# Kernel tuning notes

Measured on AMD Instinct MI355X. Metric: run time of the kernel, lower is better.

## Reference

```python
import jax, jax.numpy as jnp
import numpy as np

B, N, E = 4, 512, 128
NODE_F, EDGE_F, DYN_F, L = 16, 8, 6, 3
TOT_F = NODE_F + DYN_F  # 22


def setup_inputs() -> dict:
    key = jax.random.key(0)
    ks = jax.random.split(key, 20)
    s = 0.05
    return {
        "node_features": jax.random.normal(ks[0], (B, N, NODE_F), jnp.float32),
        "edge_features": jax.random.normal(ks[1], (B, N, N, EDGE_F), jnp.float32),
        "W": jax.random.normal(ks[2], (B, N, N), jnp.float32),
        "assigned": jax.random.randint(ks[3], (B, N), 0, 2) > 0,
        "open_group": jax.random.randint(ks[4], (B, N), 0, 2) > 0,
        "action_mask": jax.random.randint(ks[5], (B, N), 0, 2) > 0,
        "build_limit": jax.random.uniform(ks[6], (B, 3), jnp.float32, 0.5, 2.0),
        "open_group_size": jax.random.uniform(ks[7], (B, 3), jnp.float32, 0.0, 2.0),
        "node_embed_w": jax.random.normal(ks[8], (TOT_F, E), jnp.float32) * s,
        "node_embed_b": jnp.zeros((E,), jnp.float32),
        "mp_node_w": jax.random.normal(ks[9], (L, E, E), jnp.float32) * s,
        "mp_edge_w": jax.random.normal(ks[10], (L, EDGE_F, E), jnp.float32) * s,
        "mp_weight_w": jax.random.normal(ks[11], (L, E), jnp.float32) * s,
        "mp_out_w": jax.random.normal(ks[12], (L, E, E), jnp.float32) * s,
        "mp_out_b": jnp.zeros((L, E), jnp.float32),
        "context_w": jax.random.normal(ks[13], (E, E), jnp.float32) * s,
        "key_w": jax.random.normal(ks[14], (E, E), jnp.float32) * s,
        "logit_bias": jnp.zeros((1,), jnp.float32),
    }


def _policy_logits(node_features, edge_features, W, build_limit, open_group_size,
                   node_embed_w, node_embed_b, mp_node_w, mp_edge_w, mp_weight_w,
                   mp_out_w, mp_out_b, context_w, key_w, logit_bias,
                   assigned, open_group, action_mask):
    # --- dynamic node features: [B,N,6] ---
    ratio = open_group_size / jnp.maximum(build_limit, 1e-6)  # [B,3]
    dyn = jnp.concatenate([
        assigned.astype(jnp.float32)[..., None],
        open_group.astype(jnp.float32)[..., None],
        action_mask.astype(jnp.float32)[..., None],
        jnp.broadcast_to(ratio[:, None, :], (node_features.shape[0], node_features.shape[1], 3)),
    ], axis=-1)
    x = jnp.concatenate([node_features, dyn], axis=-1)  # [B,N,22]
    h = x @ node_embed_w + node_embed_b  # [B,N,E]

    # --- edge-aware message passing, residual per layer ---
    for l in range(L):
        hi = h @ mp_node_w[l]  # [B,N,E]
        ej = jnp.einsum('bijf,fe->bije', edge_features, mp_edge_w[l])  # [B,N,N,E]
        wij = W[..., None] * mp_weight_w[l]  # [B,N,N,E]
        msg = jnp.tanh(hi[:, :, None, :] + ej + wij)  # [B,N,N,E]
        agg = msg.mean(axis=2)  # [B,N,E]
        h = h + agg @ mp_out_w[l] + mp_out_b[l]

    # --- context attention logits ---
    og = open_group.astype(jnp.float32)
    has_open = jnp.any(open_group, axis=-1, keepdims=True)  # [B,1]
    denom = jnp.maximum(og.sum(axis=-1, keepdims=True), 1.0)  # [B,1]
    group_mean = (h * og[..., None]).sum(axis=1) / denom  # [B,E]
    sep_emb = h[:, 0, :]
    context = jnp.where(has_open, group_mean, sep_emb)  # [B,E]
    query = context @ context_w  # [B,E]
    keys = h @ key_w  # [B,N,E]
    logits = jnp.einsum('be,bne->bn', query, keys) / jnp.sqrt(jnp.float32(h.shape[-1]))
    logits = logits + logit_bias[0]
    logits = jnp.where(action_mask, logits, -1e9)
    return logits


def reference(node_features, edge_features, W, assigned, open_group, action_mask,
              build_limit, open_group_size, node_embed_w, node_embed_b,
              mp_node_w, mp_edge_w, mp_weight_w, mp_out_w, mp_out_b,
              context_w, key_w, logit_bias):
    return _policy_logits(node_features, edge_features, W, build_limit, open_group_size,
                          node_embed_w, node_embed_b, mp_node_w, mp_edge_w, mp_weight_w,
                          mp_out_w, mp_out_b, context_w, key_w, logit_bias,
                          assigned, open_group, action_mask)
```

## Files before the change

kernel.cpp:

```cpp
#include <hip/hip_runtime.h>
#include <math.h>

#define BB 4
#define NN 512
#define EE 128
#define NODE_F 16
#define EDGE_F 8
#define LL 3

typedef __attribute__((ext_vector_type(8))) short bf16x8;
typedef __attribute__((ext_vector_type(4))) float f32x4;

__device__ __forceinline__ ushort bf_hi(float x) {
    uint u = __float_as_uint(x);
    return (ushort)((u + 0x7fffu + ((u >> 16) & 1u)) >> 16);
}
__device__ __forceinline__ float bf_f(ushort h) {
    return __uint_as_float(((uint)h) << 16);
}

__global__ __launch_bounds__(512) void k_rows(
    const float* __restrict__ nf,
    const float* __restrict__ ef,
    const float* __restrict__ W,
    const int*   __restrict__ assigned,
    const int*   __restrict__ open_group,
    const int*   __restrict__ action_mask,
    const float* __restrict__ build_limit,
    const float* __restrict__ open_group_size,
    const float* __restrict__ embed_w,
    const float* __restrict__ embed_b,
    const float* __restrict__ node_w,
    const float* __restrict__ edge_w,
    const float* __restrict__ weight_w,
    const float* __restrict__ out_w,
    const float* __restrict__ out_b,
    float* __restrict__ hout)
{
    const int i   = blockIdx.x;
    const int b   = blockIdx.y;
    const int t   = threadIdx.x;
    const int l   = t & 63;
    const int w   = t >> 6;
    const int row = b * NN + i;

    __shared__ bf16x8 afr[32 * 64];
    __shared__ float hsh[EE];
    __shared__ float hish[EE];
    __shared__ float aggfin[EE];
    __shared__ float xsh[24];

    if (t < NODE_F) {
        xsh[t] = nf[row * NODE_F + t];
    } else if (t == 16) {
        xsh[16] = assigned[row] ? 1.0f : 0.0f;
    } else if (t == 17) {
        xsh[17] = open_group[row] ? 1.0f : 0.0f;
    } else if (t == 18) {
        xsh[18] = action_mask[row] ? 1.0f : 0.0f;
    } else if (t < 22) {
        int k = t - 19;
        xsh[t] = open_group_size[b * 3 + k] / fmaxf(build_limit[b * 3 + k], 1e-6f);
    }

    {
        const float* efr = ef + (size_t)row * NN * EDGE_F;
        const float* Wr  = W + (size_t)row * NN;
        #pragma unroll
        for (int q = 0; q < 4; ++q) {
            const int eid = t + 512 * q;
            const int ll  = eid & 63;
            const int jt  = eid >> 6;
            const int g   = ll >> 4;
            const int jj  = jt * 16 + (ll & 15);
            bf16x8 frag;
            if (g < 3) {
                const float4 a = *(const float4*)&efr[jj * 8];
                const float4 c4 = *(const float4*)&efr[jj * 8 + 4];
                float v[8] = {a.x, a.y, a.z, a.w, c4.x, c4.y, c4.z, c4.w};
                if (g < 2) {
                    #pragma unroll
                    for (int m = 0; m < 8; ++m) frag[m] = (short)bf_hi(v[m]);
                } else {
                    #pragma unroll
                    for (int m = 0; m < 8; ++m) {
                        ushort h = bf_hi(v[m]);
                        frag[m] = (short)bf_hi(v[m] - bf_f(h));
                    }
                }
            } else {
                float wv = Wr[jj];
                ushort h = bf_hi(wv);
                ushort lo = bf_hi(wv - bf_f(h));
                frag = (bf16x8){(short)h, (short)h, (short)lo, 0, 0, 0, 0, 0};
            }
            afr[eid] = frag;
        }
    }
    __syncthreads();

    if (t < EE) {
        float h0 = embed_b[t];
        #pragma unroll
        for (int k = 0; k < 22; ++k)
            h0 = fmaf(xsh[k], embed_w[k * EE + t], h0);
        hsh[t] = h0;
    }

    const float c  = 2.8853900817779268f;
    const int  le  = l & 15;
    const int  g   = l >> 4;
    const int  eN  = w * 16 + le;

    for (int lay = 0; lay < LL; ++lay) {
        __syncthreads();

        if (t < EE) {
            const float* nw = node_w + lay * EE * EE + t;
            float hp = 0.0f;
            #pragma unroll 8
            for (int k = 0; k < EE; ++k)
                hp = fmaf(hsh[k], nw[k * EE], hp);
            hish[t] = c * hp;
        }

        bf16x8 bfrag;
        if (g == 3) {
            float x = c * weight_w[lay * EE + eN];
            ushort h = bf_hi(x);
            ushort lo = bf_hi(x - bf_f(h));
            bfrag = (bf16x8){(short)h, (short)lo, (short)h, 0, 0, 0, 0, 0};
        } else {
            const float* ewp = edge_w + lay * EDGE_F * EE + eN;
            if (g == 1) {
                #pragma unroll
                for (int m = 0; m < 8; ++m) {
                    float x = c * ewp[m * EE];
                    ushort h = bf_hi(x);
                    bfrag[m] = (short)bf_hi(x - bf_f(h));
                }
            } else {
                #pragma unroll
                for (int m = 0; m < 8; ++m)
                    bfrag[m] = (short)bf_hi(c * ewp[m * EE]);
            }
        }
        __syncthreads();

        const float hq = hish[eN];
        const f32x4 cin = {hq, hq, hq, hq};

        f32x4 rsum = {0.0f, 0.0f, 0.0f, 0.0f};
        #pragma unroll 4
        for (int jt = 0; jt < 32; ++jt) {
            bf16x8 a = afr[jt * 64 + l];
            f32x4 acc = __builtin_amdgcn_mfma_f32_16x16x32_bf16(a, bfrag, cin, 0, 0, 0);
            #pragma unroll
            for (int r = 0; r < 4; ++r) {
                float ex = __builtin_amdgcn_exp2f(acc[r]);
                rsum[r] += __builtin_amdgcn_rcpf(ex + 1.0f);
            }
        }
        float s = (rsum[0] + rsum[1]) + (rsum[2] + rsum[3]);
        s += __shfl_xor(s, 16);
        s += __shfl_xor(s, 32);
        if (l < 16)
            aggfin[w * 16 + le] = 1.0f - s * (1.0f / 256.0f);
        __syncthreads();

        if (t < EE) {
            const float* ow = out_w + lay * EE * EE + t;
            float hn = hsh[t] + out_b[lay * EE + t];
            #pragma unroll 8
            for (int k = 0; k < EE; ++k)
                hn = fmaf(aggfin[k], ow[k * EE], hn);
            hsh[t] = hn;
        }
    }

    __syncthreads();
    if (t < EE) hout[(size_t)row * EE + t] = hsh[t];
}

__global__ __launch_bounds__(1024) void k_tail(
    const float* __restrict__ hbuf,
    const int*   __restrict__ open_group,
    const float* __restrict__ context_w,
    const float* __restrict__ key_w,
    const int*   __restrict__ action_mask,
    const float* __restrict__ logit_bias,
    float* __restrict__ out)
{
    const int b = blockIdx.x;
    const int t = threadIdx.x;
    const int e = t & 127;
    const int s = t >> 7;

    __shared__ float gmsh[8][EE];
    __shared__ float cntsh[8];
    __shared__ float csh[EE];
    __shared__ float qsh[EE];
    __shared__ float qksh[EE];

    const float* hb = hbuf + (size_t)b * NN * EE;

    float gm = 0.0f, cnt = 0.0f;
    const int n0 = s * 64;
    #pragma unroll 4
    for (int u = 0; u < 64; ++u) {
        const int n = n0 + u;
        const float m = (float)open_group[b * NN + n];
        gm = fmaf(m, hb[(size_t)n * EE + e], gm);
        cnt += m;
    }
    gmsh[s][e] = gm;
    if (e == 0) cntsh[s] = cnt;
    __syncthreads();

    if (s == 0) {
        float ca = 0.0f, ga = 0.0f;
        #pragma unroll
        for (int u = 0; u < 8; ++u) { ca += cntsh[u]; ga += gmsh[u][e]; }
        csh[e] = (ca > 0.0f) ? (ga / fmaxf(ca, 1.0f)) : hb[e];
    }
    __syncthreads();

    if (s == 0) {
        float q = 0.0f;
        #pragma unroll 8
        for (int k = 0; k < EE; ++k)
            q = fmaf(csh[k], context_w[k * EE + e], q);
        qsh[e] = q;
    }
    __syncthreads();

    if (s == 0) {
        float acc = 0.0f;
        const float* kr = key_w + e * EE;
        #pragma unroll 8
        for (int k = 0; k < EE; ++k)
            acc = fmaf(kr[k], qsh[k], acc);
        qksh[e] = acc;
    }
    __syncthreads();

    const int wid  = t >> 6;
    const int lane = t & 63;
    const float lb = logit_bias[0];

    for (int r = wid; r < NN; r += 16) {
        const float* hr = hb + (size_t)r * EE;
        float p = hr[lane] * qksh[lane] + hr[lane + 64] * qksh[lane + 64];
        #pragma unroll
        for (int off = 32; off; off >>= 1)
            p += __shfl_down(p, off);
        if (lane == 0) {
            float v = fmaf(p, 0.08838834764831845f, lb);
            out[b * NN + r] = action_mask[b * NN + r] ? v : -1000000000.0f;
        }
    }
}

extern "C" void kernel_launch(void* const* d_in, const int* in_sizes, int n_in,
                              void* d_out, int out_size, void* d_ws, size_t ws_size,
                              hipStream_t stream) {
    const float* nf         = (const float*)d_in[0];
    const float* ef         = (const float*)d_in[1];
    const float* W          = (const float*)d_in[2];
    const int*   assigned   = (const int*)d_in[3];
    const int*   open_group = (const int*)d_in[4];
    const int*   action_mask= (const int*)d_in[5];
    const float* build_limit= (const float*)d_in[6];
    const float* og_size    = (const float*)d_in[7];
    const float* embed_w    = (const float*)d_in[8];
    const float* embed_b    = (const float*)d_in[9];
    const float* node_w     = (const float*)d_in[10];
    const float* edge_w     = (const float*)d_in[11];
    const float* weight_w   = (const float*)d_in[12];
    const float* out_w      = (const float*)d_in[13];
    const float* out_b      = (const float*)d_in[14];
    const float* context_w  = (const float*)d_in[15];
    const float* key_w      = (const float*)d_in[16];
    const float* logit_bias = (const float*)d_in[17];

    float* hbuf = (float*)d_ws;

    dim3 grid_rows(NN, BB, 1);
    k_rows<<<grid_rows, 512, 0, stream>>>(nf, ef, W, assigned, open_group,
        action_mask, build_limit, og_size, embed_w, embed_b, node_w, edge_w,
        weight_w, out_w, out_b, hbuf);

    k_tail<<<BB, 1024, 0, stream>>>(hbuf, open_group, context_w, key_w,
        action_mask, logit_bias, (float*)d_out);
}
```

Measured before the change: 243.2 us.

## Split per-row matvecs across all warps and batch four sigmoid reciprocals into one

The two 128x128 matvecs per layer (node_w and out_w) now run on all 512 threads instead of 128. Each thread group handles a 32-wide slice of k, and the partial sums are reduced through shared memory, which cuts the serial dependency chain that left most warps idle. The sigmoid accumulation now combines four 1/(1+e) terms into a single rational expression, so it needs one rcp per MFMA output instead of four. It clamps the exponent at 30 to avoid overflow in the product. The price is an extra __syncthreads, additional shared memory, and a slight change in numerics.

Measured after the change: 248.8 us. 2.3% more time.

```diff
diff --git a/kernel.cpp b/kernel.cpp
--- a/kernel.cpp
+++ b/kernel.cpp
@@ -42,11 +42,14 @@
     const int t   = threadIdx.x;
     const int l   = t & 63;
     const int w   = t >> 6;
+    const int e   = t & 127;
+    const int ks  = t >> 7;
     const int row = b * NN + i;
 
     __shared__ bf16x8 afr[32 * 64];
     __shared__ float hsh[EE];
-    __shared__ float hish[EE];
+    __shared__ float hipart[4][EE];
+    __shared__ float opart[4][EE];
     __shared__ float aggfin[EE];
     __shared__ float xsh[24];
 
@@ -115,13 +118,13 @@
     for (int lay = 0; lay < LL; ++lay) {
         __syncthreads();
 
-        if (t < EE) {
-            const float* nw = node_w + lay * EE * EE + t;
+        {
+            const float* nw = node_w + lay * EE * EE + ks * 32 * EE + e;
             float hp = 0.0f;
             #pragma unroll 8
-            for (int k = 0; k < EE; ++k)
-                hp = fmaf(hsh[k], nw[k * EE], hp);
-            hish[t] = c * hp;
+            for (int k = 0; k < 32; ++k)
+                hp = fmaf(hsh[ks * 32 + k], nw[k * EE], hp);
+            hipart[ks][e] = hp;
         }
 
         bf16x8 bfrag;
@@ -147,34 +150,45 @@
         }
         __syncthreads();
 
-        const float hq = hish[eN];
+        const float hq = c * ((hipart[0][eN] + hipart[1][eN])
+                            + (hipart[2][eN] + hipart[3][eN]));
         const f32x4 cin = {hq, hq, hq, hq};
 
-        f32x4 rsum = {0.0f, 0.0f, 0.0f, 0.0f};
+        float rsum = 0.0f;
         #pragma unroll 4
         for (int jt = 0; jt < 32; ++jt) {
             bf16x8 a = afr[jt * 64 + l];
             f32x4 acc = __builtin_amdgcn_mfma_f32_16x16x32_bf16(a, bfrag, cin, 0, 0, 0);
-            #pragma unroll
-            for (int r = 0; r < 4; ++r) {
-                float ex = __builtin_amdgcn_exp2f(acc[r]);
-                rsum[r] += __builtin_amdgcn_rcpf(ex + 1.0f);
-            }
-        }
-        float s = (rsum[0] + rsum[1]) + (rsum[2] + rsum[3]);
+            float A0 = __builtin_amdgcn_exp2f(fminf(acc[0], 30.0f)) + 1.0f;
+            float A1 = __builtin_amdgcn_exp2f(fminf(acc[1], 30.0f)) + 1.0f;
+            float A2 = __builtin_amdgcn_exp2f(fminf(acc[2], 30.0f)) + 1.0f;
+            float A3 = __builtin_amdgcn_exp2f(fminf(acc[3], 30.0f)) + 1.0f;
+            float P01 = A0 * A1, S01 = A0 + A1;
+            float P23 = A2 * A3, S23 = A2 + A3;
+            float Nn = fmaf(P01, S23, S01 * P23);
+            float Dd = P01 * P23;
+            rsum = fmaf(Nn, __builtin_amdgcn_rcpf(Dd), rsum);
+        }
+        float s = rsum;
         s += __shfl_xor(s, 16);
         s += __shfl_xor(s, 32);
         if (l < 16)
             aggfin[w * 16 + le] = 1.0f - s * (1.0f / 256.0f);
         __syncthreads();
 
+        {
+            const float* ow = out_w + lay * EE * EE + ks * 32 * EE + e;
+            float op = 0.0f;
+            #pragma unroll 8
+            for (int k = 0; k < 32; ++k)
+                op = fmaf(aggfin[ks * 32 + k], ow[k * EE], op);
+            opart[ks][e] = op;
+        }
+        __syncthreads();
+
         if (t < EE) {
-            const float* ow = out_w + lay * EE * EE + t;
-            float hn = hsh[t] + out_b[lay * EE + t];
-            #pragma unroll 8
-            for (int k = 0; k < EE; ++k)
-                hn = fmaf(aggfin[k], ow[k * EE], hn);
-            hsh[t] = hn;
+            hsh[t] = hsh[t] + out_b[lay * EE + t]
+                   + (opart[0][t] + opart[1][t]) + (opart[2][t] + opart[3][t]);
         }
     }
 
```
